# Kernel optimization log

Hardware: AMD Instinct MI355X
Metric: run time of the kernel (lower is better)

Reference implementation:

```python
import jax, jax.numpy as jnp
from jax import lax
import numpy as np
import math

IN_CH = 256
SCALES = [128, 256, 512]
ASPECT = [0.5, 1.0, 2.0]
NUM_A = len(SCALES) * len(ASPECT)  # 9
PRENMS_TOPK = 2000
RPN_TOPK = 1000
NMS_TH = 0.7
MIN_SIZE = 16.0
IMG_H = IMG_W = 1600
FEAT_H = FEAT_W = 200
BBOX_CLIP = math.log(1000.0 / 16.0)  # standard dw/dh clamp in box decoding


def setup_inputs() -> dict:
    key = jax.random.key(0)
    ks = jax.random.split(key, 6)
    image = jax.random.normal(ks[0], (1, 3, IMG_H, IMG_W), jnp.float32)
    feat = jax.random.normal(ks[1], (1, IN_CH, FEAT_H, FEAT_W), jnp.float32)
    # params init per init_weights(): normal(std=0.01), zero bias
    conv_w = jax.random.normal(ks[2], (IN_CH, IN_CH, 3, 3), jnp.float32) * 0.01
    conv_b = jnp.zeros((IN_CH,), jnp.float32)
    cls_w = jax.random.normal(ks[3], (NUM_A, IN_CH, 1, 1), jnp.float32) * 0.01
    cls_b = jnp.zeros((NUM_A,), jnp.float32)
    reg_w = jax.random.normal(ks[4], (NUM_A * 4, IN_CH, 1, 1), jnp.float32) * 0.01
    reg_b = jnp.zeros((NUM_A * 4,), jnp.float32)
    return dict(image=image, feat=feat, conv_w=conv_w, conv_b=conv_b,
                cls_w=cls_w, cls_b=cls_b, reg_w=reg_w, reg_b=reg_b)


def _conv(x, w, b, pad):
    y = lax.conv_general_dilated(x, w, (1, 1), [(pad, pad), (pad, pad)],
                                 dimension_numbers=('NCHW', 'OIHW', 'NCHW'))
    return y + b[None, :, None, None]


def _generate_anchors(img_hw, feat_hw):
    # static (numpy) anchor grid, faithful to generate_anchors_
    gh, gw = feat_hw
    ih, iw = img_hw
    sh, sw = ih // gh, iw // gw
    scales = np.array(SCALES, np.float32)
    ar = np.array(ASPECT, np.float32)
    hr = np.sqrt(ar)
    wr = 1.0 / hr
    ws = (wr[:, None] * scales[None, :]).reshape(-1)
    hs = (hr[:, None] * scales[None, :]).reshape(-1)
    base = np.round(np.stack([-ws, -hs, ws, hs], axis=1) / 2.0)  # (A,4)
    sx = np.arange(gw, dtype=np.float32) * sw
    sy = np.arange(gh, dtype=np.float32) * sh
    yy, xx = np.meshgrid(sy, sx, indexing='ij')
    xx = xx.reshape(-1)
    yy = yy.reshape(-1)
    shifts = np.stack([xx, yy, xx, yy], axis=1)  # (H*W,4)
    anchors = (shifts[:, None, :] + base[None, :, :]).reshape(-1, 4)
    return jnp.asarray(anchors, jnp.float32)


def _apply_deltas(anchors, deltas):
    w = anchors[:, 2] - anchors[:, 0]
    h = anchors[:, 3] - anchors[:, 1]
    cx = anchors[:, 0] + 0.5 * w
    cy = anchors[:, 1] + 0.5 * h
    dx, dy = deltas[:, 0], deltas[:, 1]
    dw = jnp.minimum(deltas[:, 2], BBOX_CLIP)
    dh = jnp.minimum(deltas[:, 3], BBOX_CLIP)
    pcx = dx * w + cx
    pcy = dy * h + cy
    pw = jnp.exp(dw) * w
    ph = jnp.exp(dh) * h
    return jnp.stack([pcx - 0.5 * pw, pcy - 0.5 * ph,
                      pcx + 0.5 * pw, pcy + 0.5 * ph], axis=1)


def _nms_keep(boxes, valid, thresh):
    # boxes sorted by descending score; greedy NMS via dense IoU matrix
    K = boxes.shape[0]
    area = (boxes[:, 2] - boxes[:, 0]) * (boxes[:, 3] - boxes[:, 1])
    lt = jnp.maximum(boxes[:, None, :2], boxes[None, :, :2])
    rb = jnp.minimum(boxes[:, None, 2:], boxes[None, :, 2:])
    wh = jnp.maximum(rb - lt, 0.0)
    inter = wh[..., 0] * wh[..., 1]
    iou = inter / (area[:, None] + area[None, :] - inter + 1e-9)
    idx = jnp.arange(K)

    def body(i, keep):
        sup = (iou[i] > thresh) & keep[i] & (idx > i)
        return keep & (~sup)

    return lax.fori_loop(0, K, body, valid)


def reference(image, feat, conv_w, conv_b, cls_w, cls_b, reg_w, reg_b):
    H, W = feat.shape[-2], feat.shape[-1]
    x = jax.nn.relu(_conv(feat, conv_w, conv_b, 1))          # (1,C,H,W)
    cls = _conv(x, cls_w, cls_b, 0)                          # (1,A,H,W)
    scores = cls.transpose(0, 2, 3, 1).reshape(-1)           # (H*W*A,)
    reg = _conv(x, reg_w, reg_b, 0)                          # (1,4A,H,W)
    deltas = reg.reshape(1, NUM_A, 4, H, W).transpose(0, 3, 4, 1, 2).reshape(-1, 4)
    anchors = _generate_anchors((image.shape[-2], image.shape[-1]), (H, W))
    proposals = _apply_deltas(anchors, lax.stop_gradient(deltas))  # .detach() in source

    s = jax.nn.sigmoid(scores)
    topv, topi = lax.top_k(s, PRENMS_TOPK)                   # sorted descending
    p = proposals[topi]
    ih = jnp.float32(image.shape[-2])
    iw = jnp.float32(image.shape[-1])
    p = jnp.stack([jnp.clip(p[:, 0], 0.0, iw), jnp.clip(p[:, 1], 0.0, ih),
                   jnp.clip(p[:, 2], 0.0, iw), jnp.clip(p[:, 3], 0.0, ih)], axis=1)
    valid = ((p[:, 2] - p[:, 0]) >= MIN_SIZE) & ((p[:, 3] - p[:, 1]) >= MIN_SIZE)
    sc = jnp.where(valid, topv, -1.0)                        # invalid -> score -1 (masked out)
    order = jnp.argsort(-sc)
    b = p[order]
    sc = sc[order]
    v = valid[order]
    keep = _nms_keep(b, v, NMS_TH)
    final = jnp.where(keep, sc, -1.0)
    fi = jnp.argsort(-final)[:RPN_TOPK]                      # post-NMS sort + topk
    sel = final[fi]
    out_boxes = jnp.where(sel[:, None] > 0.0, b[fi], 0.0)
    out_scores = jnp.where(sel > 0.0, sel, 0.0)
    return out_boxes, out_scores
```

## Files before the change

kernel.cpp:

```cpp
#include <hip/hip_runtime.h>
#include <math.h>

#define FH 200
#define FW 200
#define HW 40000
#define NUM_A 9
#define NANCH 360000
#define PRE_K 2000
#define OUT_K 1000
#define IMG_SZ 1600.0f
#define MIN_SZ 16.0f
#define NMS_TH 0.7f
#define BBOX_CLIP_F 4.135166556742356f

#define OFF_HIST   ((size_t)0)
#define OFF_STATE  ((size_t)1024)
#define OFF_CAND   ((size_t)1088)
#define OFF_BOXS   ((size_t)33856)
#define OFF_SCS    ((size_t)65856)
#define OFF_MASK   ((size_t)73856)
#define OFF_DIAG   ((size_t)585856)
#define OFF_AWH    ((size_t)602240)
#define OFF_AWM    ((size_t)1781888)
#define OFF_AWL    ((size_t)2961536)
#define OFF_HWH    ((size_t)4141184)
#define OFF_HWM    ((size_t)4165760)
#define OFF_HWL    ((size_t)4190336)
#define OFF_LOGIT  ((size_t)4214912)
#define OFF_PH     ((size_t)18614912)
#define OFF_PM     ((size_t)39094912)
#define OFF_PL     ((size_t)59574912)
#define OFF_PROP   ((size_t)18614912)
#define OFF_SCORE  ((size_t)24374912)

typedef __attribute__((ext_vector_type(8))) short short8;
typedef __attribute__((ext_vector_type(4))) float floatx4;
#define MFMA16(a, b, c) __builtin_amdgcn_mfma_f32_16x16x32_bf16(a, b, c, 0, 0, 0)

__device__ __forceinline__ unsigned short rne_bf16(float v) {
  unsigned int bb = __float_as_uint(v);
  return (unsigned short)((bb + 0x7FFFu + ((bb >> 16) & 1u)) >> 16);
}

__device__ __forceinline__ void split3(float v, unsigned short& h,
                                       unsigned short& m, unsigned short& l) {
  h = rne_bf16(v);
  float r1 = v - __uint_as_float(((unsigned int)h) << 16);
  m = rne_bf16(r1);
  float r2 = r1 - __uint_as_float(((unsigned int)m) << 16);
  l = rne_bf16(r2);
}

__global__ __launch_bounds__(256) void prep_all(
    const float* __restrict__ feat, const float* __restrict__ w,
    const float* __restrict__ cls_w, const float* __restrict__ reg_w,
    unsigned short* __restrict__ Ph, unsigned short* __restrict__ Pm,
    unsigned short* __restrict__ Pl, uint4* __restrict__ AW_h,
    uint4* __restrict__ AW_m, uint4* __restrict__ AW_l,
    uint4* __restrict__ HwF_h, uint4* __restrict__ HwF_m,
    uint4* __restrict__ HwF_l) {
  int bx = blockIdx.x;
  int t = threadIdx.x;
  if (bx < 1256) {
    int cib = bx & 7;
    int px = (bx >> 3) * 256 + t;
    if (px >= HW) return;
    unsigned short h[32], m[32], l[32];
#pragma unroll
    for (int ci = 0; ci < 32; ++ci)
      split3(feat[(size_t)(cib * 32 + ci) * HW + px], h[ci], m[ci], l[ci]);
    size_t base = ((size_t)cib * HW + px) * 32;
    uint4* dh = (uint4*)(Ph + base);
    uint4* dm = (uint4*)(Pm + base);
    uint4* dl = (uint4*)(Pl + base);
#pragma unroll
    for (int k = 0; k < 4; ++k) {
      uint4 vh, vm, vl;
      vh.x = h[k * 8 + 0] | (h[k * 8 + 1] << 16);
      vh.y = h[k * 8 + 2] | (h[k * 8 + 3] << 16);
      vh.z = h[k * 8 + 4] | (h[k * 8 + 5] << 16);
      vh.w = h[k * 8 + 6] | (h[k * 8 + 7] << 16);
      vm.x = m[k * 8 + 0] | (m[k * 8 + 1] << 16);
      vm.y = m[k * 8 + 2] | (m[k * 8 + 3] << 16);
      vm.z = m[k * 8 + 4] | (m[k * 8 + 5] << 16);
      vm.w = m[k * 8 + 6] | (m[k * 8 + 7] << 16);
      vl.x = l[k * 8 + 0] | (l[k * 8 + 1] << 16);
      vl.y = l[k * 8 + 2] | (l[k * 8 + 3] << 16);
      vl.z = l[k * 8 + 4] | (l[k * 8 + 5] << 16);
      vl.w = l[k * 8 + 6] | (l[k * 8 + 7] << 16);
      dh[k] = vh; dm[k] = vm; dl[k] = vl;
    }
    return;
  }
  int gid = (bx - 1256) * 256 + t;
  unsigned short h[8], m[8], l[8];
  if (gid < 73728) {
    int L = gid & 63;
    int idx = gid >> 6;
    int cib = idx & 7;
    int tmp = idx >> 3;
    int tap = tmp % 9;
    int ctg = tmp / 9;
    int co = ctg * 16 + (L & 15);
    int ci0 = cib * 32 + (L >> 4) * 8;
#pragma unroll
    for (int j = 0; j < 8; ++j)
      split3(w[(size_t)co * 2304 + (ci0 + j) * 9 + tap], h[j], m[j], l[j]);
    uint4 vh, vm, vl;
    vh.x = h[0] | (h[1] << 16); vh.y = h[2] | (h[3] << 16);
    vh.z = h[4] | (h[5] << 16); vh.w = h[6] | (h[7] << 16);
    vm.x = m[0] | (m[1] << 16); vm.y = m[2] | (m[3] << 16);
    vm.z = m[4] | (m[5] << 16); vm.w = m[6] | (m[7] << 16);
    vl.x = l[0] | (l[1] << 16); vl.y = l[2] | (l[3] << 16);
    vl.z = l[4] | (l[5] << 16); vl.w = l[6] | (l[7] << 16);
    AW_h[gid] = vh; AW_m[gid] = vm; AW_l[gid] = vl;
  } else if (gid < 73728 + 1536) {
    int g2 = gid - 73728;
    int L = g2 & 63;
    int idx = g2 >> 6;
    int kb = idx & 7;
    int mt = idx >> 3;
    int mm = mt * 16 + (L & 15);
    int co0 = kb * 32 + (L >> 4) * 8;
#pragma unroll
    for (int j = 0; j < 8; ++j) {
      float v = 0.f;
      if (mm < 9) v = cls_w[mm * 256 + co0 + j];
      else if (mm < 45) v = reg_w[(mm - 9) * 256 + co0 + j];
      split3(v, h[j], m[j], l[j]);
    }
    uint4 vh, vm, vl;
    vh.x = h[0] | (h[1] << 16); vh.y = h[2] | (h[3] << 16);
    vh.z = h[4] | (h[5] << 16); vh.w = h[6] | (h[7] << 16);
    vm.x = m[0] | (m[1] << 16); vm.y = m[2] | (m[3] << 16);
    vm.z = m[4] | (m[5] << 16); vm.w = m[6] | (m[7] << 16);
    vl.x = l[0] | (l[1] << 16); vl.y = l[2] | (l[3] << 16);
    vl.z = l[4] | (l[5] << 16); vl.w = l[6] | (l[7] << 16);
    HwF_h[g2] = vh; HwF_m[g2] = vm; HwF_l[g2] = vl;
  }
}

__global__ __launch_bounds__(256, 3) void conv_mfma(
    const unsigned short* __restrict__ Ph, const unsigned short* __restrict__ Pm,
    const unsigned short* __restrict__ Pl, const uint4* __restrict__ AW_h,
    const uint4* __restrict__ AW_m, const uint4* __restrict__ AW_l,
    const uint4* __restrict__ HwF_h, const uint4* __restrict__ HwF_m,
    const uint4* __restrict__ HwF_l, const float* __restrict__ bias,
    float* __restrict__ logits) {
  __shared__ alignas(16) unsigned short smem[26112];
  const int t = threadIdx.x;
  const int L = t & 63, wv = t >> 6;
  const int q = L >> 4, nl = L & 15;
  const int w0 = blockIdx.x * 16;
  const int h0 = blockIdx.y * 8;
  const int cb = blockIdx.z;

  floatx4 acc[2][8];
#pragma unroll
  for (int ct = 0; ct < 2; ++ct)
#pragma unroll
    for (int r = 0; r < 8; ++r) acc[ct][r] = (floatx4)0.f;

  unsigned short* flh = smem;
  unsigned short* flm = smem + 7200;
  unsigned short* fll = smem + 14400;

  uint4 pv[9];

#define PREFETCH(CIB)                                                        \
  {                                                                          \
    _Pragma("unroll")                                                        \
    for (int j = 0; j < 9; ++j) {                                            \
      const int p = j / 3;                                                   \
      const int c = (j % 3) * 256 + t;                                       \
      uint4 v; v.x = v.y = v.z = v.w = 0u;                                   \
      if (c < 720) {                                                         \
        int rr = (int)((unsigned)c / 72u);                                   \
        int rem = c - rr * 72;                                               \
        int cc = rem >> 2, q16 = rem & 3;                                    \
        int gr = h0 - 1 + rr, gc = w0 - 1 + cc;                              \
        if ((unsigned)gr < (unsigned)FH && (unsigned)gc < (unsigned)FW) {    \
          const unsigned short* pp = (p == 0) ? Ph : (p == 1) ? Pm : Pl;     \
          v = *(const uint4*)(pp +                                           \
                ((size_t)((CIB) * HW + gr * FW + gc) * 32 + q16 * 8));       \
        }                                                                    \
      }                                                                      \
      pv[j] = v;                                                             \
    }                                                                        \
  }

#define STORE_STAGE()                                                        \
  {                                                                          \
    _Pragma("unroll")                                                        \
    for (int j = 0; j < 9; ++j) {                                            \
      const int p = j / 3;                                                   \
      const int c = (j % 3) * 256 + t;                                       \
      if (c < 720) {                                                         \
        int rr = (int)((unsigned)c / 72u);                                   \
        int rem = c - rr * 72;                                               \
        int cc = rem >> 2, q16 = rem & 3;                                    \
        *(uint4*)(smem + p * 7200 + rr * 720 + cc * 40 + q16 * 8) = pv[j];   \
      }                                                                      \
    }                                                                        \
  }

  PREFETCH(0);
  STORE_STAGE();
  __syncthreads();

  for (int cib = 0; cib < 8; ++cib) {
    if (cib < 7) PREFETCH(cib + 1);
    __builtin_amdgcn_s_setprio(1);
    const int ctg0 = cb * 8 + wv * 2;
    for (int kh = 0; kh < 3; ++kh) {
      for (int kw = 0; kw < 3; ++kw) {
        const int tap = kh * 3 + kw;
        const int abase = ((ctg0 * 9 + tap) * 8 + cib) * 64 + L;
        const int abase1 = abase + 9 * 8 * 64;
        short8 ah0 = ((const short8*)AW_h)[abase];
        short8 am0 = ((const short8*)AW_m)[abase];
        short8 al0 = ((const short8*)AW_l)[abase];
        short8 ah1 = ((const short8*)AW_h)[abase1];
        short8 am1 = ((const short8*)AW_m)[abase1];
        short8 al1 = ((const short8*)AW_l)[abase1];
        const int cbase = (nl + kw) * 40 + q * 8;
#pragma unroll
        for (int r = 0; r < 8; ++r) {
          const int off = (r + kh) * 720 + cbase;
          short8 bh = *(const short8*)(flh + off);
          short8 bm = *(const short8*)(flm + off);
          short8 bl = *(const short8*)(fll + off);
          acc[0][r] = MFMA16(ah0, bh, acc[0][r]);
          acc[0][r] = MFMA16(ah0, bm, acc[0][r]);
          acc[0][r] = MFMA16(am0, bh, acc[0][r]);
          acc[0][r] = MFMA16(ah0, bl, acc[0][r]);
          acc[0][r] = MFMA16(am0, bm, acc[0][r]);
          acc[0][r] = MFMA16(al0, bh, acc[0][r]);
          acc[1][r] = MFMA16(ah1, bh, acc[1][r]);
          acc[1][r] = MFMA16(ah1, bm, acc[1][r]);
          acc[1][r] = MFMA16(am1, bh, acc[1][r]);
          acc[1][r] = MFMA16(ah1, bl, acc[1][r]);
          acc[1][r] = MFMA16(am1, bm, acc[1][r]);
          acc[1][r] = MFMA16(al1, bh, acc[1][r]);
        }
      }
    }
    __builtin_amdgcn_s_setprio(0);
    __syncthreads();
    if (cib < 7) {
      STORE_STAGE();
      __syncthreads();
    }
  }
#undef PREFETCH
#undef STORE_STAGE

  float bv[2][4];
#pragma unroll
  for (int ct = 0; ct < 2; ++ct)
#pragma unroll
    for (int i = 0; i < 4; ++i)
      bv[ct][i] = bias[cb * 128 + (wv * 2 + ct) * 16 + q * 4 + i];

  unsigned short* xlh = smem;
  unsigned short* xlm = smem + 8704;
  unsigned short* xll = smem + 17408;

  for (int hp = 0; hp < 2; ++hp) {
    __syncthreads();
#pragma unroll
    for (int ct = 0; ct < 2; ++ct) {
#pragma unroll
      for (int rr = 0; rr < 4; ++rr) {
        int r = hp * 4 + rr;
        unsigned short xh[4], xm[4], xl_[4];
#pragma unroll
        for (int i = 0; i < 4; ++i) {
          float xv = fmaxf(acc[ct][r][i] + bv[ct][i], 0.f);
          split3(xv, xh[i], xm[i], xl_[i]);
        }
        int px_l = rr * 16 + nl;
        int co_l = (wv * 2 + ct) * 16 + q * 4;
        uint2 ph, pm, pl;
        ph.x = xh[0] | (xh[1] << 16); ph.y = xh[2] | (xh[3] << 16);
        pm.x = xm[0] | (xm[1] << 16); pm.y = xm[2] | (xm[3] << 16);
        pl.x = xl_[0] | (xl_[1] << 16); pl.y = xl_[2] | (xl_[3] << 16);
        *(uint2*)(xlh + px_l * 136 + co_l) = ph;
        *(uint2*)(xlm + px_l * 136 + co_l) = pm;
        *(uint2*)(xll + px_l * 136 + co_l) = pl;
      }
    }
    __syncthreads();
    floatx4 ha[3];
#pragma unroll
    for (int mt = 0; mt < 3; ++mt) ha[mt] = (floatx4)0.f;
    for (int ks = 0; ks < 4; ++ks) {
      const int off = (wv * 16 + nl) * 136 + ks * 32 + q * 8;
      short8 bh = *(const short8*)(xlh + off);
      short8 bm = *(const short8*)(xlm + off);
      short8 bl = *(const short8*)(xll + off);
#pragma unroll
      for (int mt = 0; mt < 3; ++mt) {
        const int hb = (mt * 8 + cb * 4 + ks) * 64 + L;
        short8 hh = ((const short8*)HwF_h)[hb];
        short8 hm = ((const short8*)HwF_m)[hb];
        short8 hl = ((const short8*)HwF_l)[hb];
        ha[mt] = MFMA16(hh, bh, ha[mt]);
        ha[mt] = MFMA16(hh, bm, ha[mt]);
        ha[mt] = MFMA16(hm, bh, ha[mt]);
        ha[mt] = MFMA16(hh, bl, ha[mt]);
        ha[mt] = MFMA16(hm, bm, ha[mt]);
        ha[mt] = MFMA16(hl, bh, ha[mt]);
      }
    }
    int gr = h0 + hp * 4 + wv;
    int gc = w0 + nl;
    if (gc < FW) {
      float* lp = logits + ((size_t)cb * HW + (size_t)(gr * FW + gc)) * 45;
#pragma unroll
      for (int mt = 0; mt < 3; ++mt)
#pragma unroll
        for (int i = 0; i < 4; ++i) {
          int head = mt * 16 + q * 4 + i;
          if (head < 45) lp[head] = ha[mt][i];
        }
    }
  }
}

__global__ __launch_bounds__(256) void finalize_kernel(
    const float* __restrict__ logits, const float* __restrict__ cls_b,
    const float* __restrict__ reg_b, float* __restrict__ prop,
    float* __restrict__ score, unsigned int* __restrict__ hist,
    unsigned int* __restrict__ state) {
  __shared__ unsigned int hsh[256], s1[256];
  __shared__ int lastb;
  int t = threadIdx.x;
  hsh[t] = 0u;
  __syncthreads();
  int px = blockIdx.x * 256 + t;
  if (px < HW) {
    float A[45];
    const float* lpA = logits + (size_t)px * 45;
    const float* lpB = logits + (size_t)HW * 45 + (size_t)px * 45;
#pragma unroll
    for (int i = 0; i < 45; ++i) A[i] = lpA[i] + lpB[i];
    const float scv[3] = {128.f, 256.f, 512.f};
    const float arv[3] = {0.5f, 1.f, 2.f};
    float sx = (float)(px % FW) * 8.0f;
    float sy = (float)(px / FW) * 8.0f;
#pragma unroll
    for (int a = 0; a < NUM_A; ++a) {
      int ai = a / 3, si = a % 3;
      float hr = sqrtf(arv[ai]);
      float wr = 1.0f / hr;
      float rw = nearbyintf(wr * scv[si] * 0.5f);
      float rh = nearbyintf(hr * scv[si] * 0.5f);
      float ax0 = sx - rw, ay0 = sy - rh, ax1 = sx + rw, ay1 = sy + rh;
      float aw = ax1 - ax0, ah = ay1 - ay0;
      float cx = ax0 + 0.5f * aw, cy = ay0 + 0.5f * ah;
      float dx = A[9 + a * 4 + 0] + reg_b[a * 4 + 0];
      float dy = A[9 + a * 4 + 1] + reg_b[a * 4 + 1];
      float dw = fminf(A[9 + a * 4 + 2] + reg_b[a * 4 + 2], BBOX_CLIP_F);
      float dh = fminf(A[9 + a * 4 + 3] + reg_b[a * 4 + 3], BBOX_CLIP_F);
      float pcx = dx * aw + cx;
      float pcy = dy * ah + cy;
      float pw = expf(dw) * aw;
      float ph = expf(dh) * ah;
      size_t base = (size_t)(px * NUM_A + a) * 4;
      prop[base + 0] = pcx - 0.5f * pw;
      prop[base + 1] = pcy - 0.5f * ph;
      prop[base + 2] = pcx + 0.5f * pw;
      prop[base + 3] = pcy + 0.5f * ph;
      float lg = A[a] + cls_b[a];
      float sv = 1.0f / (1.0f + expf(-lg));
      score[px * NUM_A + a] = sv;
      atomicAdd(&hsh[__float_as_uint(sv) >> 24], 1u);
    }
  }
  __syncthreads();
  if (hsh[t]) atomicAdd(&hist[t], hsh[t]);
  __syncthreads();
  if (t == 0) lastb = (atomicAdd(&state[8], 1u) == gridDim.x - 1u) ? 1 : 0;
  __syncthreads();
  if (!lastb) return;
  __threadfence();
  unsigned int hv = hist[t];
  hist[t] = 0u;
  hsh[t] = hv;
  __syncthreads();
  unsigned int* A = hsh;
  unsigned int* B = s1;
  for (int off = 1; off < 256; off <<= 1) {
    B[t] = A[t] + ((t + off < 256) ? A[t + off] : 0u);
    __syncthreads();
    unsigned int* tmp = A; A = B; B = tmp;
  }
  unsigned int rem = (unsigned)PRE_K;
  unsigned int suf = A[t];
  unsigned int sufn = (t < 255) ? A[t + 1] : 0u;
  if (suf >= rem && sufn < rem) {
    state[0] = (unsigned int)t;
    state[1] = rem - sufn;
  }
}

__global__ __launch_bounds__(256) void hist_scan_kernel(
    const float* __restrict__ score, unsigned int* __restrict__ hist,
    unsigned int* __restrict__ state, unsigned int* __restrict__ ticket,
    int pass) {
  __shared__ unsigned int h[256], s1[256];
  __shared__ int lastb;
  int t = threadIdx.x;
  h[t] = 0;
  __syncthreads();
  unsigned int prefix = state[0];
  int shift = 24 - 8 * pass;
  for (int i = blockIdx.x * 256 + t; i < NANCH; i += gridDim.x * 256) {
    unsigned int key = __float_as_uint(score[i]);
    if ((key >> (32 - 8 * pass)) == prefix)
      atomicAdd(&h[(key >> shift) & 255u], 1u);
  }
  __syncthreads();
  if (h[t]) atomicAdd(&hist[t], h[t]);
  __syncthreads();
  if (t == 0) lastb = (atomicAdd(ticket, 1u) == gridDim.x - 1u) ? 1 : 0;
  __syncthreads();
  if (!lastb) return;
  __threadfence();
  unsigned int hv = hist[t];
  hist[t] = 0u;
  h[t] = hv;
  __syncthreads();
  unsigned int* A = h;
  unsigned int* B = s1;
  for (int off = 1; off < 256; off <<= 1) {
    B[t] = A[t] + ((t + off < 256) ? A[t + off] : 0u);
    __syncthreads();
    unsigned int* tmp = A; A = B; B = tmp;
  }
  unsigned int rem = state[1];
  unsigned int suf = A[t];
  unsigned int sufn = (t < 255) ? A[t + 1] : 0u;
  if (suf >= rem && sufn < rem) {
    state[0] = (prefix << 8) | (unsigned int)t;
    state[1] = rem - sufn;
  }
}

__global__ __launch_bounds__(256) void collect_kernel(
    const float* __restrict__ score, unsigned int* __restrict__ state,
    unsigned long long* __restrict__ cand) {
  unsigned int T = state[0];
  for (int i = blockIdx.x * 256 + threadIdx.x; i < NANCH; i += gridDim.x * 256) {
    unsigned int key = __float_as_uint(score[i]);
    if (key >= T) {
      unsigned int pos = atomicAdd(&state[4], 1u);
      if (pos < 4096u)
        cand[pos] = ((unsigned long long)key << 32) |
                    (unsigned long long)(~(unsigned int)i);
    }
  }
}

__global__ __launch_bounds__(1024) void sort_gather(
    const unsigned long long* __restrict__ cand,
    const unsigned int* __restrict__ state, const float* __restrict__ prop,
    const float* __restrict__ score, float* __restrict__ boxes_s,
    float* __restrict__ sc_s) {
  __shared__ unsigned long long sk[4096];
  int t = threadIdx.x;
  unsigned int cnt = state[4];
  if (cnt > 4096u) cnt = 4096u;
  for (int e = t; e < 4096; e += 1024) sk[e] = (e < (int)cnt) ? cand[e] : 0ull;
  __syncthreads();
  for (int k = 2; k <= 4096; k <<= 1) {
    for (int j = k >> 1; j > 0; j >>= 1) {
      for (int i = t; i < 4096; i += 1024) {
        int l = i ^ j;
        if (l > i) {
          unsigned long long a = sk[i], bb = sk[l];
          bool up = ((i & k) == 0);
          bool sw = up ? (a < bb) : (a > bb);
          if (sw) { sk[i] = bb; sk[l] = a; }
        }
      }
      __syncthreads();
    }
  }
  float bx[2][4];
  float sc2[2] = {-1.f, -1.f};
  bool valid2[2] = {false, false};
#pragma unroll
  for (int s = 0; s < 2; ++s) {
    int i = t + s * 1024;
    bx[s][0] = bx[s][1] = bx[s][2] = bx[s][3] = 0.f;
    if (i < PRE_K) {
      unsigned long long v = sk[i];
      unsigned int idx = ~(unsigned int)(v & 0xFFFFFFFFull);
      float4 p = *(const float4*)(prop + (size_t)idx * 4);
      float x0 = fminf(fmaxf(p.x, 0.f), IMG_SZ);
      float y0 = fminf(fmaxf(p.y, 0.f), IMG_SZ);
      float x1 = fminf(fmaxf(p.z, 0.f), IMG_SZ);
      float y1 = fminf(fmaxf(p.w, 0.f), IMG_SZ);
      bool valid = (x1 - x0 >= MIN_SZ) && (y1 - y0 >= MIN_SZ);
      bx[s][0] = x0; bx[s][1] = y0; bx[s][2] = x1; bx[s][3] = y1;
      valid2[s] = valid;
      sc2[s] = valid ? score[idx] : -1.0f;
    }
  }
  __syncthreads();
  int* A = (int*)sk;
  int* B = A + 2048;
#pragma unroll
  for (int s = 0; s < 2; ++s) {
    int i = t + s * 1024;
    A[i] = (i < PRE_K && valid2[s]) ? 1 : 0;
  }
  __syncthreads();
  for (int off = 1; off < 2048; off <<= 1) {
#pragma unroll
    for (int s = 0; s < 2; ++s) {
      int i = t + s * 1024;
      B[i] = A[i] + ((i >= off) ? A[i - off] : 0);
    }
    __syncthreads();
    int* tmp = A; A = B; B = tmp;
  }
  int total = A[2047];
#pragma unroll
  for (int s = 0; s < 2; ++s) {
    int i = t + s * 1024;
    if (i < PRE_K) {
      int inc = A[i];
      int pos = valid2[s] ? (inc - 1) : (total + (i - inc));
      boxes_s[pos * 4 + 0] = bx[s][0];
      boxes_s[pos * 4 + 1] = bx[s][1];
      boxes_s[pos * 4 + 2] = bx[s][2];
      boxes_s[pos * 4 + 3] = bx[s][3];
      sc_s[pos] = sc2[s];
    }
  }
}

__global__ __launch_bounds__(64) void iou_kernel(
    const float* __restrict__ boxes_s, unsigned long long* __restrict__ mask,
    unsigned long long* __restrict__ diag) {
  int bi = blockIdx.y, bj = blockIdx.x;
  int t = threadIdx.x;
  __shared__ float4 cb[64];
  int jc = bj * 64 + t;
  float4 z; z.x = z.y = z.z = z.w = 0.f;
  cb[t] = (jc < PRE_K) ? *(const float4*)(boxes_s + (size_t)jc * 4) : z;
  __syncthreads();
  int i = bi * 64 + t;
  if (i >= PRE_K) return;
  float4 a = *(const float4*)(boxes_s + (size_t)i * 4);
  float areaA = (a.z - a.x) * (a.w - a.y);
  unsigned long long bits = 0ull;
  for (int jj = 0; jj < 64; ++jj) {
    int j = bj * 64 + jj;
    if (j < PRE_K && j > i) {
      float4 b = cb[jj];
      float areaB = (b.z - b.x) * (b.w - b.y);
      float ltx = fmaxf(a.x, b.x), lty = fmaxf(a.y, b.y);
      float rbx = fminf(a.z, b.z), rby = fminf(a.w, b.w);
      float w = fmaxf(rbx - ltx, 0.f), h = fmaxf(rby - lty, 0.f);
      float inter = w * h;
      float iou = inter / (areaA + areaB - inter + 1e-9f);
      if (iou > NMS_TH) bits |= (1ull << jj);
    }
  }
  mask[(size_t)i * 32 + bj] = bits;
  if (bi == bj) diag[i] = bits;
}

__global__ __launch_bounds__(256) void nms_out_kernel(
    const float* __restrict__ boxes_s, const float* __restrict__ sc_s,
    const unsigned long long* __restrict__ mask,
    const unsigned long long* __restrict__ diag, float* __restrict__ out) {
  int t = threadIdx.x;
  for (int e = t; e < (OUT_K * 4 + OUT_K); e += 256) out[e] = 0.f;
  __shared__ unsigned long long keepw[32];
  if (t < 64) {
    unsigned long long removed = 0ull;
    if (t < 32) {
      keepw[t] = 0ull;
#pragma unroll
      for (int k = 0; k < 64; ++k) {
        int idx = t * 64 + k;
        if (idx >= PRE_K || sc_s[idx] < 0.f) removed |= (1ull << k);
      }
    }
    const int w = t & 31;
    const int half = t >> 5;
    unsigned int kept = 0;
    for (int b = 0; b < 32; ++b) {
      unsigned long long d = diag[b * 64 + t];
      unsigned long long dead = __shfl(removed, b);
      unsigned long long alive = 0ull;
#pragma unroll
      for (int k = 0; k < 64; ++k) {
        unsigned long long dk = __shfl(d, k);
        if (!((dead >> k) & 1ull)) {
          alive |= (1ull << k);
          dead |= dk;
        }
      }
      if (t == 0) keepw[b] = alive;
      kept += (unsigned)__popcll(alive);
      if (kept >= (unsigned)OUT_K || b == 31) break;
      unsigned long long am = alive;
      const long long rb = (long long)b * 64;
      while (am) {
        int k0 = __ffsll(am) - 1; am &= am - 1;
        int k1 = k0, k2 = k0, k3 = k0, k4 = k0, k5 = k0, k6 = k0, k7 = k0;
        if (am) { k1 = __ffsll(am) - 1; am &= am - 1; }
        if (am) { k2 = __ffsll(am) - 1; am &= am - 1; }
        if (am) { k3 = __ffsll(am) - 1; am &= am - 1; }
        if (am) { k4 = __ffsll(am) - 1; am &= am - 1; }
        if (am) { k5 = __ffsll(am) - 1; am &= am - 1; }
        if (am) { k6 = __ffsll(am) - 1; am &= am - 1; }
        if (am) { k7 = __ffsll(am) - 1; am &= am - 1; }
        unsigned long long v0 = mask[(size_t)(rb + (half ? k1 : k0)) * 32 + w];
        unsigned long long v1 = mask[(size_t)(rb + (half ? k3 : k2)) * 32 + w];
        unsigned long long v2 = mask[(size_t)(rb + (half ? k5 : k4)) * 32 + w];
        unsigned long long v3 = mask[(size_t)(rb + (half ? k7 : k6)) * 32 + w];
        unsigned long long vv = v0 | v1 | v2 | v3;
        unsigned long long hv = __shfl(vv, w + 32);
        if (t < 32) removed |= vv | hv;
      }
    }
  }
  __syncthreads();
  __shared__ unsigned int wbase[32];
  if (t == 0) {
    unsigned int s = 0;
    for (int k = 0; k < 32; ++k) {
      wbase[k] = s;
      s += (unsigned)__popcll(keepw[k]);
    }
  }
  __syncthreads();
  for (int i = t; i < PRE_K; i += 256) {
    unsigned long long w2 = keepw[i >> 6];
    if ((w2 >> (i & 63)) & 1ull) {
      unsigned int pos =
          wbase[i >> 6] +
          (unsigned)__popcll(w2 & ((1ull << (i & 63)) - 1ull));
      if (pos < OUT_K) {
        out[pos * 4 + 0] = boxes_s[i * 4 + 0];
        out[pos * 4 + 1] = boxes_s[i * 4 + 1];
        out[pos * 4 + 2] = boxes_s[i * 4 + 2];
        out[pos * 4 + 3] = boxes_s[i * 4 + 3];
        out[OUT_K * 4 + pos] = sc_s[i];
      }
    }
  }
}

extern "C" void kernel_launch(void* const* d_in, const int* in_sizes, int n_in,
                              void* d_out, int out_size, void* d_ws,
                              size_t ws_size, hipStream_t stream) {
  const float* feat = (const float*)d_in[1];
  const float* convw = (const float*)d_in[2];
  const float* convb = (const float*)d_in[3];
  const float* clsw = (const float*)d_in[4];
  const float* clsb = (const float*)d_in[5];
  const float* regw = (const float*)d_in[6];
  const float* regb = (const float*)d_in[7];

  char* ws = (char*)d_ws;
  unsigned int* hist = (unsigned int*)(ws + OFF_HIST);
  unsigned int* state = (unsigned int*)(ws + OFF_STATE);
  unsigned long long* cand = (unsigned long long*)(ws + OFF_CAND);
  float* boxes_s = (float*)(ws + OFF_BOXS);
  float* sc_s = (float*)(ws + OFF_SCS);
  unsigned long long* mask = (unsigned long long*)(ws + OFF_MASK);
  unsigned long long* diag = (unsigned long long*)(ws + OFF_DIAG);
  uint4* AW_h = (uint4*)(ws + OFF_AWH);
  uint4* AW_m = (uint4*)(ws + OFF_AWM);
  uint4* AW_l = (uint4*)(ws + OFF_AWL);
  uint4* HwF_h = (uint4*)(ws + OFF_HWH);
  uint4* HwF_m = (uint4*)(ws + OFF_HWM);
  uint4* HwF_l = (uint4*)(ws + OFF_HWL);
  float* logits = (float*)(ws + OFF_LOGIT);
  unsigned short* Ph = (unsigned short*)(ws + OFF_PH);
  unsigned short* Pm = (unsigned short*)(ws + OFF_PM);
  unsigned short* Pl = (unsigned short*)(ws + OFF_PL);
  float* prop = (float*)(ws + OFF_PROP);
  float* score = (float*)(ws + OFF_SCORE);
  float* out = (float*)d_out;

  hipMemsetAsync(ws, 0, OFF_STATE + 64, stream);

  prep_all<<<1550, 256, 0, stream>>>(feat, convw, clsw, regw, Ph, Pm, Pl,
                                     AW_h, AW_m, AW_l, HwF_h, HwF_m, HwF_l);
  conv_mfma<<<dim3(13, 25, 2), 256, 0, stream>>>(Ph, Pm, Pl, AW_h, AW_m, AW_l,
                                                 HwF_h, HwF_m, HwF_l, convb,
                                                 logits);
  finalize_kernel<<<157, 256, 0, stream>>>(logits, clsb, regb, prop, score,
                                           hist, state);
  for (int p = 1; p < 4; ++p)
    hist_scan_kernel<<<256, 256, 0, stream>>>(score, hist, state,
                                              &state[8 + p], p);
  collect_kernel<<<256, 256, 0, stream>>>(score, state, cand);
  sort_gather<<<1, 1024, 0, stream>>>(cand, state, prop, score, boxes_s, sc_s);
  iou_kernel<<<dim3(32, 32), 64, 0, stream>>>(boxes_s, mask, diag);
  nms_out_kernel<<<1, 256, 0, stream>>>(boxes_s, sc_s, mask, diag, out);
}
```

Measured before the change: 615.3 us.

## Drop conv register prefetch, size bitonic sort adaptively, batch IOU tiles per block

The conv kernel no longer prefetches the next channel block into registers; it loads directly into shared memory between barriers, freeing registers but exposing load latency. The single-block bitonic sort runs over 2048 elements when the candidate count fits, halving barrier-bound stages. The IOU kernel packs four column tiles into one 256-thread block to cut launch and block overhead.

New measurement: 579.9 us. 1.06x faster.

```diff
diff --git a/kernel.cpp b/kernel.cpp
--- a/kernel.cpp
+++ b/kernel.cpp
@@ -165,51 +165,27 @@
   unsigned short* flm = smem + 7200;
   unsigned short* fll = smem + 14400;
 
-  uint4 pv[9];
-
-#define PREFETCH(CIB)                                                        \
-  {                                                                          \
-    _Pragma("unroll")                                                        \
-    for (int j = 0; j < 9; ++j) {                                            \
-      const int p = j / 3;                                                   \
-      const int c = (j % 3) * 256 + t;                                       \
-      uint4 v; v.x = v.y = v.z = v.w = 0u;                                   \
-      if (c < 720) {                                                         \
-        int rr = (int)((unsigned)c / 72u);                                   \
-        int rem = c - rr * 72;                                               \
-        int cc = rem >> 2, q16 = rem & 3;                                    \
-        int gr = h0 - 1 + rr, gc = w0 - 1 + cc;                              \
-        if ((unsigned)gr < (unsigned)FH && (unsigned)gc < (unsigned)FW) {    \
-          const unsigned short* pp = (p == 0) ? Ph : (p == 1) ? Pm : Pl;     \
-          v = *(const uint4*)(pp +                                           \
-                ((size_t)((CIB) * HW + gr * FW + gc) * 32 + q16 * 8));       \
-        }                                                                    \
-      }                                                                      \
-      pv[j] = v;                                                             \
-    }                                                                        \
-  }
-
-#define STORE_STAGE()                                                        \
-  {                                                                          \
-    _Pragma("unroll")                                                        \
-    for (int j = 0; j < 9; ++j) {                                            \
-      const int p = j / 3;                                                   \
-      const int c = (j % 3) * 256 + t;                                       \
-      if (c < 720) {                                                         \
-        int rr = (int)((unsigned)c / 72u);                                   \
-        int rem = c - rr * 72;                                               \
-        int cc = rem >> 2, q16 = rem & 3;                                    \
-        *(uint4*)(smem + p * 7200 + rr * 720 + cc * 40 + q16 * 8) = pv[j];   \
-      }                                                                      \
-    }                                                                        \
-  }
-
-  PREFETCH(0);
-  STORE_STAGE();
-  __syncthreads();
-
   for (int cib = 0; cib < 8; ++cib) {
-    if (cib < 7) PREFETCH(cib + 1);
+    __syncthreads();
+#pragma unroll
+    for (int j = 0; j < 9; ++j) {
+      const int p = j / 3;
+      const int c = (j % 3) * 256 + t;
+      if (c < 720) {
+        int rr = (int)((unsigned)c / 72u);
+        int rem = c - rr * 72;
+        int cc = rem >> 2, q16 = rem & 3;
+        int gr = h0 - 1 + rr, gc = w0 - 1 + cc;
+        uint4 v; v.x = v.y = v.z = v.w = 0u;
+        if ((unsigned)gr < (unsigned)FH && (unsigned)gc < (unsigned)FW) {
+          const unsigned short* pp = (p == 0) ? Ph : (p == 1) ? Pm : Pl;
+          v = *(const uint4*)(pp +
+                ((size_t)(cib * HW + gr * FW + gc) * 32 + q16 * 8));
+        }
+        *(uint4*)(smem + p * 7200 + rr * 720 + cc * 40 + q16 * 8) = v;
+      }
+    }
+    __syncthreads();
     __builtin_amdgcn_s_setprio(1);
     const int ctg0 = cb * 8 + wv * 2;
     for (int kh = 0; kh < 3; ++kh) {
@@ -246,14 +222,7 @@
       }
     }
     __builtin_amdgcn_s_setprio(0);
-    __syncthreads();
-    if (cib < 7) {
-      STORE_STAGE();
-      __syncthreads();
-    }
-  }
-#undef PREFETCH
-#undef STORE_STAGE
+  }
 
   float bv[2][4];
 #pragma unroll
@@ -474,9 +443,10 @@
   if (cnt > 4096u) cnt = 4096u;
   for (int e = t; e < 4096; e += 1024) sk[e] = (e < (int)cnt) ? cand[e] : 0ull;
   __syncthreads();
-  for (int k = 2; k <= 4096; k <<= 1) {
+  const int n = (cnt <= 2048u) ? 2048 : 4096;
+  for (int k = 2; k <= n; k <<= 1) {
     for (int j = k >> 1; j > 0; j >>= 1) {
-      for (int i = t; i < 4096; i += 1024) {
+      for (int i = t; i < n; i += 1024) {
         int l = i ^ j;
         if (l > i) {
           unsigned long long a = sk[i], bb = sk[l];
@@ -543,17 +513,21 @@
   }
 }
 
-__global__ __launch_bounds__(64) void iou_kernel(
+__global__ __launch_bounds__(256) void iou_kernel(
     const float* __restrict__ boxes_s, unsigned long long* __restrict__ mask,
     unsigned long long* __restrict__ diag) {
-  int bi = blockIdx.y, bj = blockIdx.x;
-  int t = threadIdx.x;
-  __shared__ float4 cb[64];
-  int jc = bj * 64 + t;
-  float4 z; z.x = z.y = z.z = z.w = 0.f;
-  cb[t] = (jc < PRE_K) ? *(const float4*)(boxes_s + (size_t)jc * 4) : z;
-  __syncthreads();
-  int i = bi * 64 + t;
+  __shared__ float4 cbw[4][64];
+  const int t = threadIdx.x;
+  const int wvi = t >> 6, lane = t & 63;
+  const int bj = blockIdx.x * 4 + wvi;
+  const int bi = blockIdx.y;
+  {
+    int jc = bj * 64 + lane;
+    float4 z; z.x = z.y = z.z = z.w = 0.f;
+    cbw[wvi][lane] = (jc < PRE_K) ? *(const float4*)(boxes_s + (size_t)jc * 4) : z;
+  }
+  __syncthreads();
+  int i = bi * 64 + lane;
   if (i >= PRE_K) return;
   float4 a = *(const float4*)(boxes_s + (size_t)i * 4);
   float areaA = (a.z - a.x) * (a.w - a.y);
@@ -561,7 +535,7 @@
   for (int jj = 0; jj < 64; ++jj) {
     int j = bj * 64 + jj;
     if (j < PRE_K && j > i) {
-      float4 b = cb[jj];
+      float4 b = cbw[wvi][jj];
       float areaB = (b.z - b.x) * (b.w - b.y);
       float ltx = fmaxf(a.x, b.x), lty = fmaxf(a.y, b.y);
       float rbx = fminf(a.z, b.z), rby = fminf(a.w, b.w);
@@ -706,6 +680,6 @@
                                               &state[8 + p], p);
   collect_kernel<<<256, 256, 0, stream>>>(score, state, cand);
   sort_gather<<<1, 1024, 0, stream>>>(cand, state, prop, score, boxes_s, sc_s);
-  iou_kernel<<<dim3(32, 32), 64, 0, stream>>>(boxes_s, mask, diag);
+  iou_kernel<<<dim3(8, 32), 256, 0, stream>>>(boxes_s, mask, diag);
   nms_out_kernel<<<1, 256, 0, stream>>>(boxes_s, sc_s, mask, diag, out);
 }
```
